# Optimization experiments

Hardware: AMD Instinct MI355X
Metric: run time of the kernel (lower is better)

Reference implementation:

```python
import jax, jax.numpy as jnp
import numpy as np
from jax import lax

BACKEND_IN = [512, 512, 512, 512, 256, 128]
BACKEND_OUT = [512, 512, 512, 256, 128, 64]
BN_EPS = 1e-5


def setup_inputs() -> dict:
    key = jax.random.key(0)
    ks = jax.random.split(key, 20)
    B, H, W = 8, 64, 64
    inp = {}
    inp['x'] = jax.random.normal(ks[0], (B, 512, H, W), jnp.float32)
    inp['y'] = jax.random.normal(ks[1], (B, 512), jnp.float32)
    inp['fc_w'] = jax.random.normal(ks[2], (6, 100, 512), jnp.float32) * 0.02
    inp['fc_b'] = jnp.zeros((6, 100), jnp.float32)
    for i in range(6):
        inp[f'wb{i}'] = jax.random.normal(ks[3 + i], (BACKEND_OUT[i] * 3, 100), jnp.float32) * 0.01
        inp[f'wc{i}'] = jax.random.normal(ks[9 + i], (BACKEND_IN[i] * 3, 100), jnp.float32) * 0.01
    inp['out_w'] = jax.random.normal(ks[15], (1, 64, 1, 1), jnp.float32) * 0.01
    inp['out_b'] = jnp.zeros((1,), jnp.float32)
    return inp


def _forward(x, y, fc_w, fc_b, wbs, wcs, out_w, out_b):
    B = x.shape[0]
    for i in range(6):
        # hypernetwork: Linear(512 -> 100)
        wa = y @ fc_w[i].T + fc_b[i]                    # (B, 100)
        # diag_embed + WB/WC matmul chain collapses to a 3-way contraction:
        # w[b,o,i] = sum_k WB[o,k] * wa[b,k] * WC[i,k]
        w = jnp.einsum('ok,bk,ik->boi', wbs[i], wa, wcs[i])  # (B, 3*cout, 3*cin)
        cout = wbs[i].shape[0] // 3
        cin = wcs[i].shape[0] // 3
        w = w.reshape(B, cout, cin, 3, 3)               # same row-major view as torch
        H, W = x.shape[2], x.shape[3]
        # per-sample dynamic conv == one grouped conv with groups = B
        xg = x.reshape(1, B * cin, H, W)
        wg = w.reshape(B * cout, cin, 3, 3)
        o = lax.conv_general_dilated(
            xg, wg, window_strides=(1, 1), padding=((2, 2), (2, 2)),
            rhs_dilation=(2, 2), feature_group_count=B,
            dimension_numbers=('NCHW', 'OIHW', 'NCHW'))
        x = o.reshape(B, cout, H, W)
        # BatchNorm2d (training mode, gamma=1, beta=0) + ReLU
        mean = x.mean(axis=(0, 2, 3), keepdims=True)
        var = ((x - mean) ** 2).mean(axis=(0, 2, 3), keepdims=True)
        x = jax.nn.relu((x - mean) * lax.rsqrt(var + BN_EPS))
    # 1x1 output conv (64 -> 1)
    out = jnp.einsum('bchw,oc->bohw', x, out_w[:, :, 0, 0]) + out_b.reshape(1, -1, 1, 1)
    # F.upsample(scale_factor=8), default nearest
    out = jnp.repeat(jnp.repeat(out, 8, axis=2), 8, axis=3)
    return out


def reference(x, y, fc_w, fc_b, wb0, wb1, wb2, wb3, wb4, wb5,
              wc0, wc1, wc2, wc3, wc4, wc5, out_w, out_b):
    wbs = [wb0, wb1, wb2, wb3, wb4, wb5]
    wcs = [wc0, wc1, wc2, wc3, wc4, wc5]
    return _forward(x, y, fc_w, fc_b, wbs, wcs, out_w, out_b)
```

## Files before the change

kernel.cpp:

```cpp
#include <hip/hip_runtime.h>
#include <stdint.h>

typedef __attribute__((ext_vector_type(8))) short short8;
typedef __attribute__((ext_vector_type(4))) float f32x4;
typedef __attribute__((ext_vector_type(4))) unsigned int u32x4;

struct Ptr6 { const float* p[6]; };

struct LTab {
  const unsigned short* wbh; const unsigned short* wach;
  unsigned short* wboi; unsigned short* w2;
  int cumg[7]; int cumt[7];
  int mblk[6]; int nblk[6]; int M3[6]; int N3[6]; int CINt[6]; int COUTt[6];
  long moff[6]; long coff[6]; long woff[6];
};

__device__ __forceinline__ float bf2f(unsigned short u){
  union { unsigned int i; float f; } x; x.i = ((unsigned int)u) << 16; return x.f;
}
__device__ __forceinline__ unsigned short f2bf(float f){
  union { float f; unsigned int i; } x; x.f = f;
  unsigned int r = x.i + 0x7fffu + ((x.i >> 16) & 1u);
  return (unsigned short)(r >> 16);
}

__device__ __forceinline__ void gll16(const void* g, void* l){
  __builtin_amdgcn_global_load_lds((const __attribute__((address_space(1))) void*)g,
                                   (__attribute__((address_space(3))) void*)l, 16, 0, 0);
}

__global__ void wa_kernel(const float* __restrict__ y, const float* __restrict__ fcw,
                          const float* __restrict__ fcb, float* __restrict__ wa){
  int l = blockIdx.x >> 3, b = blockIdx.x & 7;
  int k = threadIdx.x;
  if (k >= 100) return;
  const float* yr = y + b*512;
  const float* wr = fcw + (l*100 + k)*512;
  float s = 0.f;
  for (int j=0;j<512;j++) s += yr[j]*wr[j];
  wa[(l*8+b)*100 + k] = s + fcb[l*100 + k];
}

__global__ void wbh_all_kernel(Ptr6 wb, unsigned short* __restrict__ o){
  const int roff1=1536, roff2=3072, roff3=4608, roff4=5376, roff5=5760;
  int idx = blockIdx.x*256 + threadIdx.x;
  int row = idx >> 7, k = idx & 127;
  int l, r;
  if      (row < roff1){ l=0; r=row; }
  else if (row < roff2){ l=1; r=row-roff1; }
  else if (row < roff3){ l=2; r=row-roff2; }
  else if (row < roff4){ l=3; r=row-roff3; }
  else if (row < roff5){ l=4; r=row-roff4; }
  else                 { l=5; r=row-roff5; }
  const int m3[6] = {1536,1536,1536,768,384,192};
  float v = (r < m3[l] && k < 100) ? wb.p[l][r*100 + k] : 0.f;
  o[idx] = f2bf(v);
}

__global__ void wach_all_kernel(Ptr6 wc, const float* __restrict__ wa,
                                unsigned short* __restrict__ o){
  const int c1=12288, c2=24576, c3=36864, c4=49152, c5=55296;
  int idx = blockIdx.x*256 + threadIdx.x;
  int row = idx >> 7, k = idx & 127;
  int l, r, n3;
  if      (row < c1){ l=0; r=row;    n3=1536; }
  else if (row < c2){ l=1; r=row-c1; n3=1536; }
  else if (row < c3){ l=2; r=row-c2; n3=1536; }
  else if (row < c4){ l=3; r=row-c3; n3=1536; }
  else if (row < c5){ l=4; r=row-c4; n3=768; }
  else              { l=5; r=row-c5; n3=384; }
  int b = r / n3, i = r % n3;
  float v = (k < 100) ? wa[(l*8+b)*100 + k] * wc.p[l][i*100 + k] : 0.f;
  o[idx] = f2bf(v);
}

__device__ __forceinline__ void wgen_body(
    const unsigned short* __restrict__ wbh, const unsigned short* __restrict__ wach,
    unsigned short* __restrict__ wboi, int M3, int N3, int m0, int n0, int b,
    unsigned short* At, unsigned short* Bt){
  const int t = threadIdx.x;
  const unsigned short* As = wbh + (size_t)m0*128;
  const unsigned short* Bs = wach + ((size_t)b*N3 + n0)*128;
  #pragma unroll
  for (int j=0;j<8;j++){
    int c = j*256 + t;
    int row = c >> 4, q = c & 15;
    *(u32x4*)&At[row*136 + q*8] = *(const u32x4*)&As[row*128 + q*8];
    *(u32x4*)&Bt[row*136 + q*8] = *(const u32x4*)&Bs[row*128 + q*8];
  }
  __syncthreads();
  const int wv = t >> 6, lane = t & 63;
  const int wm = (wv >> 1)*64, wn = (wv & 1)*64;
  const int lr = lane & 15, lkg = lane >> 4, lk8 = lkg*8;
  f32x4 acc[4][4];
  #pragma unroll
  for (int i=0;i<4;i++) for (int j=0;j<4;j++) acc[i][j] = (f32x4){0,0,0,0};
  #pragma unroll
  for (int kc=0;kc<4;kc++){
    short8 a[4], bv[4];
    #pragma unroll
    for (int mi=0;mi<4;mi++) a[mi] = *(const short8*)&At[(wm+mi*16+lr)*136 + kc*32 + lk8];
    #pragma unroll
    for (int ni=0;ni<4;ni++) bv[ni] = *(const short8*)&Bt[(wn+ni*16+lr)*136 + kc*32 + lk8];
    #pragma unroll
    for (int mi=0;mi<4;mi++)
      #pragma unroll
      for (int ni=0;ni<4;ni++)
        acc[mi][ni] = __builtin_amdgcn_mfma_f32_16x16x32_bf16(a[mi], bv[ni], acc[mi][ni], 0,0,0);
  }
  #pragma unroll
  for (int mi=0;mi<4;mi++)
    #pragma unroll
    for (int ni=0;ni<4;ni++)
      #pragma unroll
      for (int r=0;r<4;r++){
        int o = m0 + wm + mi*16 + lkg*4 + r;
        int i = n0 + wn + ni*16 + lr;
        if (o < M3) wboi[((size_t)b*M3 + o)*N3 + i] = f2bf(acc[mi][ni][r]);
      }
}

__global__ __launch_bounds__(256) void wgen_all_kernel(LTab tab){
  __shared__ unsigned short At[128*136];
  __shared__ unsigned short Bt[128*136];
  int bid = blockIdx.x;
  int l = 0;
  #pragma unroll
  for (int i=1;i<6;i++) if (bid >= tab.cumg[i]) l = i;
  int rem = bid - tab.cumg[l];
  int mb = rem % tab.mblk[l];
  int r2 = rem / tab.mblk[l];
  int nb = r2 % tab.nblk[l];
  int b  = r2 / tab.nblk[l];
  wgen_body(tab.wbh + tab.moff[l]*128, tab.wach + tab.coff[l]*128,
            tab.wboi + tab.woff[l], tab.M3[l], tab.N3[l], mb*128, nb*128, b, At, Bt);
}

__global__ __launch_bounds__(256) void wgen_kernel(
    const unsigned short* __restrict__ wbh, const unsigned short* __restrict__ wach,
    unsigned short* __restrict__ wboi, int M3, int N3){
  __shared__ unsigned short At[128*136];
  __shared__ unsigned short Bt[128*136];
  wgen_body(wbh, wach, wboi, M3, N3, blockIdx.x*128, blockIdx.y*128, blockIdx.z, At, Bt);
}

__device__ __forceinline__ void wtr_body(
    const unsigned short* __restrict__ wboi, unsigned short* __restrict__ W2,
    int CIN, int COUT, int co, int b, unsigned short* buf){
  const int t = threadIdx.x;
  const int n = 9*CIN;
  const unsigned short* src = wboi + ((size_t)b*3*COUT + 3*co)*(size_t)(3*CIN);
  for (int i = t*8; i < n; i += 2048) *(u32x4*)&buf[i] = *(const u32x4*)&src[i];
  __syncthreads();
  const int nch = n >> 3;
  const int cpr = CIN >> 3;
  for (int idx = t; idx < nch; idx += 256){
    int tap = idx / cpr, cig = idx - tap*cpr;
    short8 v;
    #pragma unroll
    for (int j=0;j<8;j++) v[j] = (short)buf[(cig*8+j)*9 + tap];
    *(short8*)&W2[(((size_t)(b*9 + tap)*COUT) + co)*CIN + cig*8] = v;
  }
}

__global__ void wtr_all_kernel(LTab tab){
  __shared__ unsigned short buf[9*512];
  int bid = blockIdx.x;
  int l = 0;
  #pragma unroll
  for (int i=1;i<6;i++) if (bid >= tab.cumt[i]) l = i;
  int rem = bid - tab.cumt[l];
  int co = rem % tab.COUTt[l];
  int b  = rem / tab.COUTt[l];
  wtr_body(tab.wboi + tab.woff[l], tab.w2 + tab.woff[l], tab.CINt[l], tab.COUTt[l], co, b, buf);
}

__global__ void wtr_kernel(const unsigned short* __restrict__ wboi, unsigned short* __restrict__ W2,
                           int CIN, int COUT){
  __shared__ unsigned short buf[9*512];
  wtr_body(wboi, W2, CIN, COUT, blockIdx.x % COUT, blockIdx.x / COUT, buf);
}

__global__ void castx_kernel(const float* __restrict__ x, unsigned short* __restrict__ act){
  __shared__ float tile[64][65];
  int bid = blockIdx.x;
  int ct = bid & 7; int hp = (bid >> 3) % 68; int b = bid / 544;
  int c0 = ct * 64;
  int t = threadIdx.x;
  unsigned short* orow = act + ((size_t)(b*68 + hp)*68)*512;
  if (hp < 2 || hp >= 66){
    for (int idx = t; idx < 68*64; idx += 256){
      int wp = idx >> 6, c = idx & 63;
      orow[wp*512 + c0 + c] = 0;
    }
    return;
  }
  int h = hp - 2;
  for (int idx = t; idx < 64*64; idx += 256){
    int r = idx >> 6, w = idx & 63;
    tile[r][w] = x[((size_t)(b*512 + c0 + r)*64 + h)*64 + w];
  }
  __syncthreads();
  for (int idx = t; idx < 68*64; idx += 256){
    int wp = idx >> 6, c = idx & 63;
    float v = (wp < 2 || wp >= 66) ? 0.f : tile[c][wp-2];
    orow[wp*512 + c0 + c] = f2bf(v);
  }
}

template<int CIN, int COUT>
__global__ __launch_bounds__(256, 2) void conv_kernel(
    const unsigned short* __restrict__ act, const unsigned short* __restrict__ W2,
    float* __restrict__ cbuf, float* __restrict__ partial){
  __shared__ unsigned short Al[9*256*8];
  __shared__ unsigned short Pl[20*20*4*8];
  const int co0 = blockIdx.x * 64;
  const int h0 = (blockIdx.y >> 2) * 16;
  const int w0 = (blockIdx.y & 3) * 16;
  const int b = blockIdx.z;
  const int t = threadIdx.x;
  const int wv = t >> 6, lane = t & 63;
  const int lr = lane & 15, lkg = lane >> 4;

  const unsigned short* actb = act + (size_t)b*68*68*CIN;
  const unsigned short* wb = W2 + (size_t)b*9*COUT*CIN;

  const unsigned short* ga[16];
  #pragma unroll
  for (int j=0;j<16;j++){
    int id = wv*16 + j;
    if (id < 36){
      int tap = id >> 2, q = id & 3;
      int co = lane ^ q;
      ga[j] = &wb[((size_t)(tap*COUT + co0 + co))*CIN + q*8];
    } else if (id < 61){
      int s = (id-36)*64 + lane;
      int pp = s >> 2;
      int ph = pp/20, pw = pp - ph*20;
      int q = (s&3) ^ ((pw>>1)&3);
      ga[j] = &actb[(size_t)((h0+ph)*68 + (w0+pw))*CIN + q*8];
    } else {
      ga[j] = nullptr;
    }
  }

  f32x4 acc[4][4];
  #pragma unroll
  for (int i=0;i<4;i++) for (int j=0;j<4;j++) acc[i][j] = (f32x4){0,0,0,0};

  for (int cs = 0; cs < CIN/32; ++cs){
    #pragma unroll
    for (int j=0;j<16;j++){
      int id = wv*16 + j;
      if (id < 61){
        unsigned short* lp = (id < 36) ? &Al[id*512] : &Pl[(id-36)*512];
        gll16((const void*)ga[j], (void*)lp);
        ga[j] += 32;
      }
    }
    __syncthreads();
    #pragma unroll
    for (int kh=0;kh<3;kh++){
      #pragma unroll
      for (int kw=0;kw<3;kw++){
        const int tap = kh*3 + kw;
        short8 a[4], bv[4];
        #pragma unroll
        for (int mi=0;mi<4;mi++)
          a[mi] = *(const short8*)&Al[(tap*256 + lkg*64 + ((mi*16+lr)^lkg))*8];
        #pragma unroll
        for (int ni=0;ni<4;ni++){
          int pr = wv*4 + ni + 2*kh;
          int pc = lr + 2*kw;
          bv[ni] = *(const short8*)&Pl[((pr*20+pc)*4 + (lkg ^ ((pc>>1)&3)))*8];
        }
        #pragma unroll
        for (int mi=0;mi<4;mi++)
          #pragma unroll
          for (int ni=0;ni<4;ni++)
            acc[mi][ni] = __builtin_amdgcn_mfma_f32_16x16x32_bf16(a[mi], bv[ni], acc[mi][ni], 0,0,0);
      }
    }
    __syncthreads();
  }
  float* ob = cbuf + (size_t)b*64*64*COUT;
  #pragma unroll
  for (int mi=0;mi<4;mi++){
    int co = co0 + mi*16 + lkg*4;
    #pragma unroll
    for (int ni=0;ni<4;ni++){
      int hh = h0 + wv*4 + ni;
      int ww = w0 + lr;
      *(f32x4*)&ob[(size_t)(hh*64 + ww)*COUT + co] = acc[mi][ni];
    }
  }
  float ps[4][4], pq[4][4];
  #pragma unroll
  for (int mi=0;mi<4;mi++)
    #pragma unroll
    for (int r=0;r<4;r++){ ps[mi][r]=0.f; pq[mi][r]=0.f; }
  #pragma unroll
  for (int mi=0;mi<4;mi++)
    #pragma unroll
    for (int ni=0;ni<4;ni++)
      #pragma unroll
      for (int r=0;r<4;r++){
        float v = acc[mi][ni][r];
        ps[mi][r] += v; pq[mi][r] += v*v;
      }
  #pragma unroll
  for (int m=1;m<16;m<<=1)
    #pragma unroll
    for (int mi=0;mi<4;mi++)
      #pragma unroll
      for (int r=0;r<4;r++){
        ps[mi][r] += __shfl_xor(ps[mi][r], m);
        pq[mi][r] += __shfl_xor(pq[mi][r], m);
      }
  if (lr == 0){
    const int tile = (blockIdx.y*8 + blockIdx.z)*4 + wv;
    #pragma unroll
    for (int mi=0;mi<4;mi++)
      #pragma unroll
      for (int r=0;r<4;r++){
        int co = co0 + mi*16 + lkg*4 + r;
        ((float2*)partial)[co*512 + tile] = make_float2(ps[mi][r], pq[mi][r]);
      }
  }
}

__global__ void bnfin_kernel(const float* __restrict__ partial, float* __restrict__ bnmr, int C){
  int lane = threadIdx.x & 31, ch8 = threadIdx.x >> 5;
  int c = blockIdx.x*8 + ch8;
  if (c >= C) return;
  const float2* p = (const float2*)partial + (size_t)c*512;
  float s=0.f, q=0.f;
  for (int tl=lane; tl<512; tl+=32){
    float2 v = p[tl];
    s += v.x; q += v.y;
  }
  #pragma unroll
  for (int m=1;m<32;m<<=1){
    s += __shfl_xor(s, m);
    q += __shfl_xor(q, m);
  }
  if (lane == 0){
    const float inv_n = 1.f/32768.f;
    float mean = s*inv_n;
    float var = q*inv_n - mean*mean;
    bnmr[c] = mean;
    bnmr[512 + c] = rsqrtf(var + 1e-5f);
  }
}

__global__ void bnapply_kernel(const float* __restrict__ cbuf, const float* __restrict__ bnmr,
                               unsigned short* __restrict__ actout, int lc){
  const int C = 1 << lc;
  const int bid = blockIdx.x;
  const int hp = bid % 68, b = bid / 68;
  const int t = threadIdx.x;
  unsigned short* orow = actout + (((size_t)(b*68 + hp))*68 << lc);
  const bool hb = (hp < 2) || (hp >= 66);
  const int n = 68 << lc;
  for (int idx = t; idx < n; idx += 256){
    int wp = idx >> lc, c = idx & (C-1);
    float v = 0.f;
    if (!hb && wp >= 2 && wp < 66){
      float xx = cbuf[((((size_t)b*64 + (hp-2))*64 + (wp-2)) << lc) + c];
      float z = (xx - bnmr[c]) * bnmr[512 + c];
      v = z > 0.f ? z : 0.f;
    }
    orow[idx] = f2bf(v);
  }
}

__global__ void convup_kernel(const unsigned short* __restrict__ act, const float* __restrict__ ow,
                              const float* __restrict__ ob, float* __restrict__ out){
  int idx = blockIdx.x*256 + threadIdx.x;
  int b = idx >> 12, p = idx & 4095;
  int h = p >> 6, w = p & 63;
  const unsigned short* ar = act + (((size_t)(b*68 + h+2))*68 + (w+2))*64;
  float s = 0.f;
  #pragma unroll
  for (int c=0;c<64;c++) s += bf2f(ar[c]) * ow[c];
  s += ob[0];
  f32x4 v = {s,s,s,s};
  float* o = out + (((size_t)b*512 + h*8)*512) + w*8;
  #pragma unroll
  for (int rr=0;rr<8;rr++){
    *(f32x4*)(o + (size_t)rr*512) = v;
    *(f32x4*)(o + (size_t)rr*512 + 4) = v;
  }
}

extern "C" void kernel_launch(void* const* d_in, const int* in_sizes, int n_in,
                              void* d_out, int out_size, void* d_ws, size_t ws_size,
                              hipStream_t stream){
  const float* x   = (const float*)d_in[0];
  const float* y   = (const float*)d_in[1];
  const float* fcw = (const float*)d_in[2];
  const float* fcb = (const float*)d_in[3];
  Ptr6 wbp, wcp;
  bool dictOrder = (in_sizes[10] == 76800);
  for (int i=0;i<6;i++){
    if (dictOrder){ wbp.p[i] = (const float*)d_in[4+2*i]; wcp.p[i] = (const float*)d_in[5+2*i]; }
    else          { wbp.p[i] = (const float*)d_in[4+i];   wcp.p[i] = (const float*)d_in[10+i]; }
  }
  const float* ow  = (const float*)d_in[16];
  const float* obp = (const float*)d_in[17];
  float* out = (float*)d_out;

  static const int CIN[6]  = {512,512,512,512,256,128};
  static const int COUT[6] = {512,512,512,256,128,64};
  static const int MPAD[6] = {1536,1536,1536,768,384,256};
  static const int LC[6]   = {9,9,9,8,7,6};
  static const long MOFF[6] = {0,1536,3072,4608,5376,5760};
  static const long COFF[6] = {0,12288,24576,36864,49152,55296};
  static const long WOFF[6] = {0,18874368,37748736,56623104,66060288,68419584};

  const size_t actBytes  = (size_t)8*68*68*512*2;
  const size_t cbufBytes = (size_t)8*64*64*512*4;
  const size_t wAllBytes = (size_t)69009408*2;
  const size_t w2OneBytes= (size_t)18874368*2;
  const size_t partBytes = (size_t)512*512*2*4;

  char* ws = (char*)d_ws; size_t off = 0;
  auto alloc = [&](size_t bytes)->void*{ void* p = ws + off; off += (bytes + 255) & ~(size_t)255; return p; };

  size_t needBatched = 0;
  {
    size_t o2 = 0;
    auto a2 = [&](size_t b){ o2 += (b + 255) & ~(size_t)255; };
    a2(actBytes); a2(actBytes); a2(cbufBytes); a2(wAllBytes);
    a2(6*8*100*4); a2((size_t)6016*128*2); a2((size_t)58368*128*2); a2(partBytes); a2(1024*4);
    needBatched = o2;
  }
  const bool batched = (ws_size >= needBatched);

  unsigned short* actA = (unsigned short*)alloc(actBytes);
  unsigned short* actB = (unsigned short*)alloc(actBytes);
  float* cbuf = (float*)alloc(cbufBytes);
  unsigned short* W2all = nullptr; unsigned short* W2one = nullptr; unsigned short* wboi = nullptr;
  if (batched){
    W2all = (unsigned short*)alloc(wAllBytes);
    wboi  = (unsigned short*)ws;
  } else {
    W2one = (unsigned short*)alloc(w2OneBytes);
    wboi  = (unsigned short*)cbuf;
  }
  float* wa = (float*)alloc(6*8*100*4);
  unsigned short* wbh = (unsigned short*)alloc((size_t)6016*128*2);
  unsigned short* wach = (unsigned short*)alloc((size_t)58368*128*2);
  float* partial = (float*)alloc(partBytes);
  float* bnmr = (float*)alloc(1024*4);

  wa_kernel<<<48, 128, 0, stream>>>(y, fcw, fcb, wa);
  wbh_all_kernel<<<6016*128/256, 256, 0, stream>>>(wbp, wbh);
  wach_all_kernel<<<58368*128/256, 256, 0, stream>>>(wcp, wa, wach);

  if (batched){
    LTab tab;
    tab.wbh = wbh; tab.wach = wach; tab.wboi = wboi; tab.w2 = W2all;
    int gsz[6], tsz[6];
    for (int l=0;l<6;l++){
      tab.mblk[l] = MPAD[l]/128; tab.nblk[l] = 3*CIN[l]/128;
      tab.M3[l] = 3*COUT[l]; tab.N3[l] = 3*CIN[l];
      tab.CINt[l] = CIN[l]; tab.COUTt[l] = COUT[l];
      tab.moff[l] = MOFF[l]; tab.coff[l] = COFF[l]; tab.woff[l] = WOFF[l];
      gsz[l] = tab.mblk[l]*tab.nblk[l]*8; tsz[l] = 8*COUT[l];
    }
    tab.cumg[0] = 0; tab.cumt[0] = 0;
    for (int l=0;l<6;l++){ tab.cumg[l+1] = tab.cumg[l] + gsz[l]; tab.cumt[l+1] = tab.cumt[l] + tsz[l]; }
    wgen_all_kernel<<<tab.cumg[6], 256, 0, stream>>>(tab);
    wtr_all_kernel<<<tab.cumt[6], 256, 0, stream>>>(tab);
  }

  castx_kernel<<<8*68*8, 256, 0, stream>>>(x, actA);

  unsigned short* ain = actA; unsigned short* aout = actB;
  for (int l=0;l<6;l++){
    const unsigned short* W2l;
    if (batched){
      W2l = W2all + WOFF[l];
    } else {
      int M3 = 3*COUT[l], N3 = 3*CIN[l];
      wgen_kernel<<<dim3(MPAD[l]/128, N3/128, 8), 256, 0, stream>>>(
          wbh + (size_t)MOFF[l]*128, wach + (size_t)COFF[l]*128, wboi, M3, N3);
      wtr_kernel<<<8*COUT[l], 256, 0, stream>>>(wboi, W2one, CIN[l], COUT[l]);
      W2l = W2one;
    }
    switch(l){
      case 0: case 1: case 2:
        conv_kernel<512,512><<<dim3(8,16,8),256,0,stream>>>(ain, W2l, cbuf, partial); break;
      case 3:
        conv_kernel<512,256><<<dim3(4,16,8),256,0,stream>>>(ain, W2l, cbuf, partial); break;
      case 4:
        conv_kernel<256,128><<<dim3(2,16,8),256,0,stream>>>(ain, W2l, cbuf, partial); break;
      case 5:
        conv_kernel<128,64><<<dim3(1,16,8),256,0,stream>>>(ain, W2l, cbuf, partial); break;
    }
    bnfin_kernel<<<COUT[l]/8, 256, 0, stream>>>(partial, bnmr, COUT[l]);
    bnapply_kernel<<<8*68, 256, 0, stream>>>(cbuf, bnmr, aout, LC[l]);
    unsigned short* tmp = ain; ain = aout; aout = tmp;
  }
  convup_kernel<<<(8*4096)/256, 256, 0, stream>>>(ain, ow, obp, out);
}
```

Before: 1.169 ms.

## Repack dynamic conv weights into per-chunk tiled layout for contiguous loads

Changes the weight transpose kernel to emit a layout indexed by (batch, 32-channel chunk, tap, quad, cout, 8) with the XOR swizzle baked in, handling 8 output channels per block. The conv kernel's weight loads for each K-chunk then read 64 consecutive 16-byte vectors instead of rows strided by CIN, which should improve global load coalescing. The transpose kernel uses a larger shared buffer and fewer blocks, so its occupancy and store pattern change.

```diff
diff --git a/kernel.cpp b/kernel.cpp
--- a/kernel.cpp
+++ b/kernel.cpp
@@ -144,41 +144,55 @@
   wgen_body(wbh, wach, wboi, M3, N3, blockIdx.x*128, blockIdx.y*128, blockIdx.z, At, Bt);
 }
 
-__device__ __forceinline__ void wtr_body(
-    const unsigned short* __restrict__ wboi, unsigned short* __restrict__ W2,
-    int CIN, int COUT, int co, int b, unsigned short* buf){
+__device__ __forceinline__ void wtr3_body(
+    const unsigned short* __restrict__ wboi, unsigned short* __restrict__ W3,
+    int CIN, int COUT, int cog, int b, unsigned short* buf){
   const int t = threadIdx.x;
   const int n = 9*CIN;
-  const unsigned short* src = wboi + ((size_t)b*3*COUT + 3*co)*(size_t)(3*CIN);
-  for (int i = t*8; i < n; i += 2048) *(u32x4*)&buf[i] = *(const u32x4*)&src[i];
+  const int stride = 9*CIN + 8;
+  const int cpr = n >> 3;
+  const int NCS = CIN >> 5;
+  for (int idx = t; idx < 8*cpr; idx += 256){
+    int co_r = idx / cpr, off = idx - co_r*cpr;
+    const unsigned short* src = wboi + ((size_t)b*3*COUT + 3*(cog*8+co_r))*(size_t)(3*CIN);
+    *(u32x4*)&buf[co_r*stride + off*8] = *(const u32x4*)&src[off*8];
+  }
   __syncthreads();
-  const int nch = n >> 3;
-  const int cpr = CIN >> 3;
-  for (int idx = t; idx < nch; idx += 256){
-    int tap = idx / cpr, cig = idx - tap*cpr;
+  const int total = 9*NCS*4*8;
+  for (int idx = t; idx < total; idx += 256){
+    int co_in = idx & 7;
+    int trip = idx >> 3;
+    int q = trip & 3;
+    int tcs = trip >> 2;
+    int tap = tcs % 9;
+    int cs  = tcs / 9;
+    int ci0 = cs*32 + q*8;
     short8 v;
     #pragma unroll
-    for (int j=0;j<8;j++) v[j] = (short)buf[(cig*8+j)*9 + tap];
-    *(short8*)&W2[(((size_t)(b*9 + tap)*COUT) + co)*CIN + cig*8] = v;
+    for (int e=0;e<8;e++) v[e] = (short)buf[co_in*stride + (ci0+e)*9 + tap];
+    size_t dst = ((((size_t)(b*NCS + cs)*9 + tap)*4 + q)*COUT + (cog*8 + (co_in^q)))*8;
+    *(short8*)&W3[dst] = v;
   }
 }
 
 __global__ void wtr_all_kernel(LTab tab){
-  __shared__ unsigned short buf[9*512];
+  __shared__ unsigned short buf[8*(9*512+8)];
   int bid = blockIdx.x;
   int l = 0;
   #pragma unroll
   for (int i=1;i<6;i++) if (bid >= tab.cumt[i]) l = i;
   int rem = bid - tab.cumt[l];
-  int co = rem % tab.COUTt[l];
-  int b  = rem / tab.COUTt[l];
-  wtr_body(tab.wboi + tab.woff[l], tab.w2 + tab.woff[l], tab.CINt[l], tab.COUTt[l], co, b, buf);
-}
-
-__global__ void wtr_kernel(const unsigned short* __restrict__ wboi, unsigned short* __restrict__ W2,
+  int ng = tab.COUTt[l] >> 3;
+  int cog = rem % ng;
+  int b  = rem / ng;
+  wtr3_body(tab.wboi + tab.woff[l], tab.w2 + tab.woff[l], tab.CINt[l], tab.COUTt[l], cog, b, buf);
+}
+
+__global__ void wtr_kernel(const unsigned short* __restrict__ wboi, unsigned short* __restrict__ W3,
                            int CIN, int COUT){
-  __shared__ unsigned short buf[9*512];
-  wtr_body(wboi, W2, CIN, COUT, blockIdx.x % COUT, blockIdx.x / COUT, buf);
+  __shared__ unsigned short buf[8*(9*512+8)];
+  int ng = COUT >> 3;
+  wtr3_body(wboi, W3, CIN, COUT, blockIdx.x % ng, blockIdx.x / ng, buf);
 }
 
 __global__ void castx_kernel(const float* __restrict__ x, unsigned short* __restrict__ act){
@@ -210,7 +224,7 @@
 
 template<int CIN, int COUT>
 __global__ __launch_bounds__(256, 2) void conv_kernel(
-    const unsigned short* __restrict__ act, const unsigned short* __restrict__ W2,
+    const unsigned short* __restrict__ act, const unsigned short* __restrict__ W3,
     float* __restrict__ cbuf, float* __restrict__ partial){
   __shared__ unsigned short Al[9*256*8];
   __shared__ unsigned short Pl[20*20*4*8];
@@ -223,7 +237,7 @@
   const int lr = lane & 15, lkg = lane >> 4;
 
   const unsigned short* actb = act + (size_t)b*68*68*CIN;
-  const unsigned short* wb = W2 + (size_t)b*9*COUT*CIN;
+  const unsigned short* w3b = W3 + (size_t)b*9*COUT*CIN;
 
   const unsigned short* ga[16];
   #pragma unroll
@@ -231,8 +245,7 @@
     int id = wv*16 + j;
     if (id < 36){
       int tap = id >> 2, q = id & 3;
-      int co = lane ^ q;
-      ga[j] = &wb[((size_t)(tap*COUT + co0 + co))*CIN + q*8];
+      ga[j] = &w3b[((((size_t)tap)*4 + q)*COUT + co0 + lane)*8];
     } else if (id < 61){
       int s = (id-36)*64 + lane;
       int pp = s >> 2;
@@ -248,6 +261,7 @@
   #pragma unroll
   for (int i=0;i<4;i++) for (int j=0;j<4;j++) acc[i][j] = (f32x4){0,0,0,0};
 
+  const size_t aStep = (size_t)288*COUT;
   for (int cs = 0; cs < CIN/32; ++cs){
     #pragma unroll
     for (int j=0;j<16;j++){
@@ -255,7 +269,7 @@
       if (id < 61){
         unsigned short* lp = (id < 36) ? &Al[id*512] : &Pl[(id-36)*512];
         gll16((const void*)ga[j], (void*)lp);
-        ga[j] += 32;
+        ga[j] += (id < 36) ? aStep : 32;
       }
     }
     __syncthreads();
@@ -440,12 +454,12 @@
   unsigned short* actA = (unsigned short*)alloc(actBytes);
   unsigned short* actB = (unsigned short*)alloc(actBytes);
   float* cbuf = (float*)alloc(cbufBytes);
-  unsigned short* W2all = nullptr; unsigned short* W2one = nullptr; unsigned short* wboi = nullptr;
+  unsigned short* W3all = nullptr; unsigned short* W3one = nullptr; unsigned short* wboi = nullptr;
   if (batched){
-    W2all = (unsigned short*)alloc(wAllBytes);
+    W3all = (unsigned short*)alloc(wAllBytes);
     wboi  = (unsigned short*)ws;
   } else {
-    W2one = (unsigned short*)alloc(w2OneBytes);
+    W3one = (unsigned short*)alloc(w2OneBytes);
     wboi  = (unsigned short*)cbuf;
   }
   float* wa = (float*)alloc(6*8*100*4);
@@ -460,14 +474,15 @@
 
   if (batched){
     LTab tab;
-    tab.wbh = wbh; tab.wach = wach; tab.wboi = wboi; tab.w2 = W2all;
+    tab.wbh = wbh; tab.wach = wach; tab.wboi = wboi; tab.w2 = W3all;
     int gsz[6], tsz[6];
     for (int l=0;l<6;l++){
       tab.mblk[l] = MPAD[l]/128; tab.nblk[l] = 3*CIN[l]/128;
       tab.M3[l] = 3*COUT[l]; tab.N3[l] = 3*CIN[l];
       tab.CINt[l] = CIN[l]; tab.COUTt[l] = COUT[l];
       tab.moff[l] = MOFF[l]; tab.coff[l] = COFF[l]; tab.woff[l] = WOFF[l];
-      gsz[l] = tab.mblk[l]*tab.nblk[l]*8; tsz[l] = 8*COUT[l];
+      gsz[l] = tab.mblk[l]*tab.nblk[l]*8;
+      tsz[l] = COUT[l];
     }
     tab.cumg[0] = 0; tab.cumt[0] = 0;
     for (int l=0;l<6;l++){ tab.cumg[l+1] = tab.cumg[l] + gsz[l]; tab.cumt[l+1] = tab.cumt[l] + tsz[l]; }
@@ -479,25 +494,25 @@
 
   unsigned short* ain = actA; unsigned short* aout = actB;
   for (int l=0;l<6;l++){
-    const unsigned short* W2l;
+    const unsigned short* W3l;
     if (batched){
-      W2l = W2all + WOFF[l];
+      W3l = W3all + WOFF[l];
     } else {
       int M3 = 3*COUT[l], N3 = 3*CIN[l];
       wgen_kernel<<<dim3(MPAD[l]/128, N3/128, 8), 256, 0, stream>>>(
           wbh + (size_t)MOFF[l]*128, wach + (size_t)COFF[l]*128, wboi, M3, N3);
-      wtr_kernel<<<8*COUT[l], 256, 0, stream>>>(wboi, W2one, CIN[l], COUT[l]);
-      W2l = W2one;
+      wtr_kernel<<<COUT[l], 256, 0, stream>>>(wboi, W3one, CIN[l], COUT[l]);
+      W3l = W3one;
     }
     switch(l){
       case 0: case 1: case 2:
-        conv_kernel<512,512><<<dim3(8,16,8),256,0,stream>>>(ain, W2l, cbuf, partial); break;
+        conv_kernel<512,512><<<dim3(8,16,8),256,0,stream>>>(ain, W3l, cbuf, partial); break;
       case 3:
-        conv_kernel<512,256><<<dim3(4,16,8),256,0,stream>>>(ain, W2l, cbuf, partial); break;
+        conv_kernel<512,256><<<dim3(4,16,8),256,0,stream>>>(ain, W3l, cbuf, partial); break;
       case 4:
-        conv_kernel<256,128><<<dim3(2,16,8),256,0,stream>>>(ain, W2l, cbuf, partial); break;
+        conv_kernel<256,128><<<dim3(2,16,8),256,0,stream>>>(ain, W3l, cbuf, partial); break;
       case 5:
-        conv_kernel<128,64><<<dim3(1,16,8),256,0,stream>>>(ain, W2l, cbuf, partial); break;
+        conv_kernel<128,64><<<dim3(1,16,8),256,0,stream>>>(ain, W3l, cbuf, partial); break;
     }
     bnfin_kernel<<<COUT[l]/8, 256, 0, stream>>>(partial, bnmr, COUT[l]);
     bnapply_kernel<<<8*68, 256, 0, stream>>>(cbuf, bnmr, aout, LC[l]);
```

Result: faster. 1.076 ms (-7.9%).
